# Performance work log

Hardware: AMD Instinct MI355X
Metric: run time of the kernel (lower is better)

## Reference

```python
import jax, jax.numpy as jnp
import numpy as np

K = 8      # neighbors (from __init__ default k=8)
EPS = 1e-5 # BatchNorm1d default eps


def conv1x1(x, w, b):
    # x: (B,C,N), w: (O,C), b: (O,) -> (B,O,N)
    return jnp.einsum('bcn,oc->bon', x, w) + b[None, :, None]


def batchnorm(x, g, be):
    # training-mode BatchNorm1d: stats over (B, N) per channel
    m = x.mean(axis=(0, 2), keepdims=True)
    v = x.var(axis=(0, 2), keepdims=True)
    return g[None, :, None] * (x - m) * jax.lax.rsqrt(v + EPS) + be[None, :, None]


def block(x, w, b, g, be):
    return jax.nn.relu(batchnorm(conv1x1(x, w, b), g, be))


def setup_inputs() -> dict:
    key = jax.random.key(0)
    ks = jax.random.split(key, 24)
    B, N = 16, 4096
    rn = lambda k, s, sc=0.1: jax.random.normal(k, s, jnp.float32) * sc
    ones_n = lambda k, s: jnp.ones(s, jnp.float32) + rn(k, s, 0.01)
    return {
        'points': jax.random.normal(ks[0], (B, N, 3), jnp.float32),
        'w1': rn(ks[1], (64, 3)),   'b1': rn(ks[2], (64,)),
        'g1': ones_n(ks[3], (64,)), 'be1': rn(ks[4], (64,)),
        'w3': rn(ks[5], (512, 64)), 'b3': rn(ks[6], (512,)),
        'g3': ones_n(ks[7], (512,)), 'be3': rn(ks[8], (512,)),
        'hw1': rn(ks[9], (512, 1088)), 'hb1': rn(ks[10], (512,)),
        'hg1': ones_n(ks[11], (512,)), 'hbe1': rn(ks[12], (512,)),
        'hw2': rn(ks[13], (256, 512)), 'hb2': rn(ks[14], (256,)),
        'hg2': ones_n(ks[15], (256,)), 'hbe2': rn(ks[16], (256,)),
        'hw3': rn(ks[17], (128, 256)), 'hb3': rn(ks[18], (128,)),
        'hg3': ones_n(ks[19], (128,)), 'hbe3': rn(ks[20], (128,)),
        'hw4': rn(ks[21], (6, 128)), 'hb4': rn(ks[22], (6,)),
    }


def reference(points, w1, b1, g1, be1, w3, b3, g3, be3,
              hw1, hb1, hg1, hbe1, hw2, hb2, hg2, hbe2,
              hw3, hb3, hg3, hbe3, hw4, hb4):
    B, N, _ = points.shape
    # brute-force KNN (squared L2, ascending -> top_k on -dist)
    x2 = jnp.sum(points * points, axis=-1)                     # (B,N)
    dist = x2[:, :, None] + x2[:, None, :] \
        - 2.0 * jnp.einsum('bnd,bmd->bnm', points, points)      # (B,N,N)
    idx = jax.lax.top_k(-dist, K)[1]                           # (B,N,K) int32

    p = points.transpose(0, 2, 1)                              # (B,3,N)
    l_feat = block(p, w1, b1, g1, be1)                         # (B,64,N)
    x = block(l_feat, w3, b3, g3, be3)                         # (B,512,N)
    x_t = x.transpose(0, 2, 1)                                 # (B,N,512)

    # Faithful to the original's gather bug:
    # out[b,n,k,c] = x_t[b, idx[b,n,k], k]  (independent of c since K<512)
    vals = jnp.take_along_axis(x_t[:, :, :K], idx, axis=1)     # (B,N,K)
    m = vals.max(axis=2)                                       # (B,N)
    local_features = jnp.broadcast_to(m[:, None, :], (B, 512, N))

    global_feat = jnp.broadcast_to(x.max(axis=2, keepdims=True), (B, 512, N))
    h = jnp.concatenate([local_features, l_feat, global_feat], axis=1)  # (B,1088,N)
    h = block(h, hw1, hb1, hg1, hbe1)
    h = block(h, hw2, hb2, hg2, hbe2)
    h = block(h, hw3, hb3, hg3, hbe3)
    h = conv1x1(h, hw4, hb4)                                   # (B,6,N)
    return h.transpose(0, 2, 1)                                # (B,N,6)
```

## Files before the change

### kernel.cpp

```cpp
#include <hip/hip_runtime.h>
#include <hip/hip_bf16.h>
#include <math.h>

typedef __attribute__((ext_vector_type(8))) short short8;
typedef __attribute__((ext_vector_type(16))) float f32x16;

__device__ inline f32x16 mfma32(short8 a, short8 b, f32x16 c) {
    return __builtin_amdgcn_mfma_f32_32x32x16_bf16(a, b, c, 0, 0, 0);
}

__device__ inline void bsplit(float x, ushort& h, ushort& l) {
    __hip_bfloat16 bh = __float2bfloat16(x);
    float hf = __bfloat162float(bh);
    __hip_bfloat16 bl = __float2bfloat16(x - hf);
    h = *reinterpret_cast<ushort*>(&bh);
    l = *reinterpret_cast<ushort*>(&bl);
}

__device__ inline float unmap_f(unsigned int mp) {
    unsigned int db = mp ^ (0x80000000u | (unsigned int)((int)(~mp) >> 31));
    return __uint_as_float(db);
}

__global__ void k_wsplit_all(
    const float* __restrict__ w3s, const float* __restrict__ hw1,
    const float* __restrict__ hw2, const float* __restrict__ hw3,
    const float* __restrict__ hw4,
    ushort* __restrict__ w3h, ushort* __restrict__ w3l,
    ushort* __restrict__ w1eh, ushort* __restrict__ w1el,
    ushort* __restrict__ w2h, ushort* __restrict__ w2l,
    ushort* __restrict__ wh3h, ushort* __restrict__ wh3l,
    ushort* __restrict__ w4h, ushort* __restrict__ w4l) {
    int i = blockIdx.x * 256 + threadIdx.x;
    const float* src; int rs, co, Ms, K, base; ushort *hi, *lo;
    if (i < 32768)       { src = w3s; rs = 64;   co = 0;   Ms = 512; K = 64;  hi = w3h;  lo = w3l;  base = 0; }
    else if (i < 65536)  { src = hw1; rs = 1088; co = 512; Ms = 512; K = 64;  hi = w1eh; lo = w1el; base = 32768; }
    else if (i < 196608) { src = hw2; rs = 512;  co = 0;   Ms = 256; K = 512; hi = w2h;  lo = w2l;  base = 65536; }
    else if (i < 229376) { src = hw3; rs = 256;  co = 0;   Ms = 128; K = 256; hi = wh3h; lo = wh3l; base = 196608; }
    else if (i < 233472) { src = hw4; rs = 128;  co = 0;   Ms = 6;   K = 128; hi = w4h;  lo = w4l;  base = 229376; }
    else return;
    int li = i - base;
    int o = li / K, k = li - o * K;
    float x = (o < Ms) ? src[(size_t)o * rs + co + k] : 0.f;
    ushort h, l;
    bsplit(x, h, l);
    hi[li] = h; lo[li] = l;
}

__global__ void k_stats1(const float* __restrict__ pts, const float* __restrict__ w1,
                         const float* __restrict__ b1, float* __restrict__ part1) {
    __shared__ float sw[256];
    __shared__ float wred[2][4][64];
    int t = threadIdx.x;
    if (t < 192) sw[t] = w1[t];
    if (t < 64) sw[192 + t] = b1[t];
    __syncthreads();
    int g = blockIdx.x * 256 + t;
    float p0 = pts[g*3], p1 = pts[g*3+1], p2 = pts[g*3+2];
    int lane = t & 63, wv = t >> 6;
    for (int c = 0; c < 64; c++) {
        float y = fmaf(sw[c*3+2], p2, fmaf(sw[c*3+1], p1, fmaf(sw[c*3], p0, sw[192+c])));
        float s = y, q = y * y;
        #pragma unroll
        for (int o = 32; o > 0; o >>= 1) { s += __shfl_down(s, o); q += __shfl_down(q, o); }
        if (lane == 0) { wred[0][wv][c] = s; wred[1][wv][c] = q; }
    }
    __syncthreads();
    if (t < 64) {
        float s = wred[0][0][t] + wred[0][1][t] + wred[0][2][t] + wred[0][3][t];
        float q = wred[1][0][t] + wred[1][1][t] + wred[1][2][t] + wred[1][3][t];
        part1[blockIdx.x * 128 + t] = s;
        part1[blockIdx.x * 128 + 64 + t] = q;
    }
}

__global__ void k_fin(const float* __restrict__ part, int count, int stride, int sqoff,
                      const float* __restrict__ g, const float* __restrict__ be,
                      float* __restrict__ sout, float* __restrict__ tout) {
    int c = blockIdx.x, t = threadIdx.x;
    float s = 0.f, q = 0.f;
    for (int w = t; w < count; w += 256) { s += part[(size_t)w*stride + c]; q += part[(size_t)w*stride + sqoff + c]; }
    __shared__ float rs[4], rq[4];
    int lane = t & 63, wv = t >> 6;
    #pragma unroll
    for (int o = 32; o > 0; o >>= 1) { s += __shfl_down(s, o); q += __shfl_down(q, o); }
    if (lane == 0) { rs[wv] = s; rq[wv] = q; }
    __syncthreads();
    if (t == 0) {
        s = rs[0] + rs[1] + rs[2] + rs[3];
        q = rq[0] + rq[1] + rq[2] + rq[3];
        float mean = s / 65536.f;
        float var = q / 65536.f - mean * mean;
        float sc = g[c] * rsqrtf(var + 1e-5f);
        sout[c] = sc;
        tout[c] = be[c] - mean * sc;
    }
}

__global__ void k_lfeat2(const float* __restrict__ pts, const float* __restrict__ w1,
                         const float* __restrict__ b1, const float* __restrict__ s1,
                         const float* __restrict__ t1, ushort* __restrict__ lfh,
                         ushort* __restrict__ lfl) {
    __shared__ float sw[256], ss[64], st[64];
    int t = threadIdx.x;
    if (t < 192) sw[t] = w1[t];
    if (t < 64) { sw[192+t] = b1[t]; ss[t] = s1[t]; st[t] = t1[t]; }
    __syncthreads();
    int g = blockIdx.x * 256 + t;
    float p0 = pts[g*3], p1 = pts[g*3+1], p2 = pts[g*3+2];
    for (int c0 = 0; c0 < 64; c0 += 8) {
        union { short8 v; ushort u[8]; } H, L;
        #pragma unroll
        for (int j = 0; j < 8; j++) {
            int c = c0 + j;
            float y = fmaf(sw[c*3+2], p2, fmaf(sw[c*3+1], p1, fmaf(sw[c*3], p0, sw[192+c])));
            float a = fmaxf(fmaf(ss[c], y, st[c]), 0.f);
            bsplit(a, H.u[j], L.u[j]);
        }
        *(short8*)(lfh + (size_t)g*64 + c0) = H.v;
        *(short8*)(lfl + (size_t)g*64 + c0) = L.v;
    }
}

template<int MODE>
__global__ __launch_bounds__(256, 2) void k_gemm64(
    const ushort* __restrict__ Bhi, const ushort* __restrict__ Blo,
    const ushort* __restrict__ Ahi, const ushort* __restrict__ Alo,
    const float* __restrict__ bias, const float* __restrict__ A1,
    const float* __restrict__ G1, const float* __restrict__ mb,
    float* __restrict__ part, float* __restrict__ y38) {
    __shared__ ushort sbh[128*64], sbl[128*64];
    __shared__ float sPb[512], sPa[512];
    int t = threadIdx.x, pb = blockIdx.x;
    int gn0 = pb * 128, b = pb >> 5;
    for (int i = t; i < 512; i += 256) {
        float bb = bias[i];
        if (MODE) bb += G1[(b<<9) + i];
        sPb[i] = bb;
        sPa[i] = MODE ? A1[i] : 0.f;
    }
    for (int it = 0; it < 4; it++) {
        int s = it*256 + t;
        int n = s >> 3, c16 = s & 7;
        int off = (c16*16) ^ ((n & 7) << 4);
        int sb8 = (it*256 + (t & 192)) * 8;
        __builtin_amdgcn_global_load_lds((const char*)Bhi + (size_t)(gn0+n)*128 + off, &sbh[sb8], 16, 0, 0);
        __builtin_amdgcn_global_load_lds((const char*)Blo + (size_t)(gn0+n)*128 + off, &sbl[sb8], 16, 0, 0);
    }
    __syncthreads();
    int lane = t & 63, wv = t >> 6, m = lane & 31, kg = lane >> 5;
    for (int ct = 0; ct < 4; ct++) {
        int ch0 = wv*128 + ct*32;
        short8 ah[4], al[4];
        #pragma unroll
        for (int ks = 0; ks < 4; ks++) {
            ah[ks] = *(const short8*)(Ahi + (size_t)(ch0+m)*64 + ks*16 + kg*8);
            al[ks] = *(const short8*)(Alo + (size_t)(ch0+m)*64 + ks*16 + kg*8);
        }
        float ssum[16] = {}, ssq[16] = {}, smx[16];
        #pragma unroll
        for (int r = 0; r < 16; r++) smx[r] = -__builtin_inff();
        for (int pt = 0; pt < 4; pt++) {
            int n = pt*32 + m;
            f32x16 acc = {};
            #pragma unroll
            for (int ks = 0; ks < 4; ks++) {
                int off = ((ks*16 + kg*8)*2) ^ ((n & 7) << 4);
                short8 bh = *(const short8*)((const char*)sbh + n*128 + off);
                short8 bl = *(const short8*)((const char*)sbl + n*128 + off);
                acc = mfma32(ah[ks], bh, acc);
                acc = mfma32(ah[ks], bl, acc);
                acc = mfma32(al[ks], bh, acc);
            }
            float mval = MODE ? mb[gn0 + n] : 0.f;
            #pragma unroll
            for (int r = 0; r < 16; r++) {
                int chr = ch0 + (r&3) + 8*(r>>2) + 4*kg;
                float v = acc[r] + sPb[chr] + (MODE ? sPa[chr]*mval : 0.f);
                ssum[r] += v; ssq[r] = fmaf(v, v, ssq[r]);
                if (MODE == 0) {
                    smx[r] = fmaxf(smx[r], v);
                    if (wv == 0 && ct == 0 && r < 4) {
                        int c8 = (r&3) + 4*kg;
                        y38[(size_t)c8*65536 + gn0 + n] = v;
                    }
                }
            }
        }
        #pragma unroll
        for (int r = 0; r < 16; r++) {
            float s = ssum[r], q = ssq[r], x = smx[r];
            #pragma unroll
            for (int o = 16; o > 0; o >>= 1) {
                s += __shfl_xor(s, o); q += __shfl_xor(q, o);
                if (MODE == 0) x = fmaxf(x, __shfl_xor(x, o));
            }
            if (m == 0) {
                int chr = ch0 + (r&3) + 8*(r>>2) + 4*kg;
                if (MODE == 0) {
                    part[(size_t)pb*1536 + chr] = s;
                    part[(size_t)pb*1536 + 512 + chr] = q;
                    part[(size_t)pb*1536 + 1024 + chr] = x;
                } else {
                    part[(size_t)pb*1024 + chr] = s;
                    part[(size_t)pb*1024 + 512 + chr] = q;
                }
            }
        }
    }
}

__global__ void k_fin3b(const float* __restrict__ part3, const float* __restrict__ s3,
                        const float* __restrict__ t3, float* __restrict__ gmaxb) {
    int b = blockIdx.x, c = threadIdx.x;
    float mx = -__builtin_inff();
    for (int i = 0; i < 32; i++) mx = fmaxf(mx, part3[(size_t)(b*32+i)*1536 + 1024 + c]);
    gmaxb[(b<<9)+c] = fmaxf(fmaf(s3[c], mx, t3[c]), 0.f);
}

__global__ void k_a1g1(const float* __restrict__ hw1, const float* __restrict__ gmaxb,
                       float* __restrict__ A1, float* __restrict__ G1) {
    __shared__ float sg[512];
    int blk = blockIdx.x, t = threadIdx.x;
    if (blk < 32) {
        int b = blk >> 1;
        for (int i = t; i < 512; i += 256) sg[i] = gmaxb[(b<<9)+i];
        __syncthreads();
        int o = (blk & 1)*256 + t;
        float s = 0.f;
        for (int c4 = 0; c4 < 128; c4++) {
            float4 w = *(const float4*)&hw1[(size_t)o*1088 + 576 + c4*4];
            s = fmaf(w.x, sg[c4*4],   s);
            s = fmaf(w.y, sg[c4*4+1], s);
            s = fmaf(w.z, sg[c4*4+2], s);
            s = fmaf(w.w, sg[c4*4+3], s);
        }
        G1[(b<<9)+o] = s;
    } else {
        int o = (blk - 32)*256 + t;
        float s = 0.f;
        for (int c4 = 0; c4 < 128; c4++) {
            float4 w = *(const float4*)&hw1[(size_t)o*1088 + c4*4];
            s += w.x; s += w.y; s += w.z; s += w.w;
        }
        A1[o] = s;
    }
}

__global__ __launch_bounds__(1024, 8)
void k_knn(const float* __restrict__ pts, const float* __restrict__ y38,
           const float* __restrict__ s3, const float* __restrict__ t3,
           float* __restrict__ mbuf) {
    __shared__ float4 sp[4096];
    int t = threadIdx.x, blk = blockIdx.x;
    int b = blk >> 5;
    int lane = t & 63, wv = t >> 6;
    const float* pb = pts + (size_t)b * 4096 * 3;
    for (int i = t; i < 4096; i += 1024) {
        float c0 = pb[i*3], c1 = pb[i*3+1], c2 = pb[i*3+2];
        float cw = __fadd_rn(__fadd_rn(__fmul_rn(c0,c0), __fmul_rn(c1,c1)), __fmul_rn(c2,c2));
        sp[i] = make_float4(c0, c1, c2, cw);
    }
    __syncthreads();
    const int NINF = 0xff800000;
    int qbase = (blk & 31) * 128 + wv * 8;
    for (int qi = 0; qi < 8; qi++) {
        int nq = qbase + qi;
        float4 qp = sp[nq];
        float q0 = qp.x, q1 = qp.y, q2 = qp.z, qx2 = qp.w;
        float sd; unsigned int si;
        {
            float4 cp = sp[lane];
            float dot = __fadd_rn(__fadd_rn(__fmul_rn(q0,cp.x), __fmul_rn(q1,cp.y)), __fmul_rn(q2,cp.z));
            float d = __fsub_rn(__fadd_rn(qx2, cp.w), __fmul_rn(2.f, dot));
            unsigned int db = __float_as_uint(d);
            unsigned int mp = db ^ (0x80000000u | (unsigned int)((int)db >> 31));
            unsigned long long key = ((unsigned long long)mp << 32) | (unsigned int)lane;
            #pragma unroll
            for (int k = 2; k <= 64; k <<= 1) {
                #pragma unroll
                for (int jj = k >> 1; jj >= 1; jj >>= 1) {
                    unsigned long long pk = __shfl_xor(key, jj);
                    bool up = ((lane & k) == 0);
                    bool lower = ((lane & jj) == 0);
                    bool keepmin = (lower == up);
                    unsigned long long mn = (pk < key) ? pk : key;
                    unsigned long long mx = (pk < key) ? key : pk;
                    key = keepmin ? mn : mx;
                }
            }
            sd = unmap_f((unsigned int)(key >> 32));
            si = (unsigned int)key;
        }
        float thr = __shfl(sd, 7);
        for (int j = 1; j < 64; j++) {
            float4 cp = sp[j*64 + lane];
            float dot = __fadd_rn(__fadd_rn(__fmul_rn(q0,cp.x), __fmul_rn(q1,cp.y)), __fmul_rn(q2,cp.z));
            float d = __fsub_rn(__fadd_rn(qx2, cp.w), __fmul_rn(2.f, dot));
            unsigned long long mask = __ballot(d < thr);
            if (mask != 0ull) {
                do {
                    int src = __ffsll(mask) - 1;
                    float db = __uint_as_float(__builtin_amdgcn_readlane(__float_as_uint(d), src));
                    unsigned int mb_ = (unsigned int)(j*64 + src);
                    float pd = __int_as_float(__builtin_amdgcn_update_dpp(
                        NINF, __float_as_int(sd), 0x111, 0xf, 0xf, false));
                    unsigned int pi = (unsigned int)__builtin_amdgcn_update_dpp(
                        0, (int)si, 0x111, 0xf, 0xf, false);
                    bool keep = (sd <= db);
                    bool pk = (pd <= db);
                    sd = keep ? sd : (pk ? db : pd);
                    si = keep ? si : (pk ? mb_ : pi);
                    mask &= (mask - 1ull);
                } while (mask != 0ull);
                thr = __shfl(sd, 7);
            }
        }
        if (lane < 8) {
            float y = y38[(size_t)lane*65536 + (b<<12) + (si & 4095)];
            float mv = fmaxf(fmaf(s3[lane], y, t3[lane]), 0.f);
            mv = fmaxf(mv, __shfl_xor(mv, 1));
            mv = fmaxf(mv, __shfl_xor(mv, 2));
            mv = fmaxf(mv, __shfl_xor(mv, 4));
            if (lane == 0) mbuf[(b<<12) + nq] = mv;
        }
    }
}

__global__ __launch_bounds__(256, 2) void k_a1w(
    const ushort* __restrict__ lfh, const ushort* __restrict__ lfl,
    const ushort* __restrict__ W1hi, const ushort* __restrict__ W1lo,
    const float* __restrict__ hb1, const float* __restrict__ A1g,
    const float* __restrict__ G1g, const float* __restrict__ mb,
    const float* __restrict__ sh1, const float* __restrict__ th1,
    ushort* __restrict__ a1hg, ushort* __restrict__ a1lg) {
    __shared__ ushort sbh[32*64], sbl[32*64];
    __shared__ ushort a1h[32*512], a1l[32*512];
    __shared__ float sP0[512], sP1[512], sSh[512];
    int t = threadIdx.x, pb = blockIdx.x;
    int gn0 = pb * 32, b = pb >> 7;
    for (int i = t; i < 512; i += 256) {
        float s = sh1[i];
        sP0[i] = fmaf(s, hb1[i] + G1g[(b<<9)+i], th1[i]);
        sP1[i] = s * A1g[i];
        sSh[i] = s;
    }
    {
        int s = t;
        int n = s >> 3, c16 = s & 7;
        int off = (c16*16) ^ ((n & 7) << 4);
        int sb8 = (t & 192) * 8;
        __builtin_amdgcn_global_load_lds((const char*)lfh + (size_t)(gn0+n)*128 + off, &sbh[sb8], 16, 0, 0);
        __builtin_amdgcn_global_load_lds((const char*)lfl + (size_t)(gn0+n)*128 + off, &sbl[sb8], 16, 0, 0);
    }
    __syncthreads();
    int lane = t & 63, wv = t >> 6, m = lane & 31, kg = lane >> 5;
    float mval = mb[gn0 + m];
    for (int ct = 0; ct < 4; ct++) {
        int ch0 = wv*128 + ct*32;
        f32x16 acc = {};
        #pragma unroll
        for (int ks = 0; ks < 4; ks++) {
            short8 ah = *(const short8*)(W1hi + (size_t)(ch0+m)*64 + ks*16 + kg*8);
            short8 al = *(const short8*)(W1lo + (size_t)(ch0+m)*64 + ks*16 + kg*8);
            int off = ((ks*16 + kg*8)*2) ^ ((m & 7) << 4);
            short8 bh = *(const short8*)((const char*)sbh + m*128 + off);
            short8 bl = *(const short8*)((const char*)sbl + m*128 + off);
            acc = mfma32(ah, bh, acc);
            acc = mfma32(ah, bl, acc);
            acc = mfma32(al, bh, acc);
        }
        #pragma unroll
        for (int q = 0; q < 4; q++) {
            ushort hs[4], ls[4];
            #pragma unroll
            for (int i = 0; i < 4; i++) {
                int r = q*4 + i;
                int chr = ch0 + i + 8*q + 4*kg;
                float a = fmaxf(fmaf(sSh[chr], acc[r], sP0[chr] + sP1[chr]*mval), 0.f);
                bsplit(a, hs[i], ls[i]);
            }
            int chb = ch0 + 8*q + 4*kg;
            int off = (chb*2) ^ ((m & 15) << 4);
            uint2 vh, vl;
            vh.x = (uint)hs[0] | ((uint)hs[1] << 16); vh.y = (uint)hs[2] | ((uint)hs[3] << 16);
            vl.x = (uint)ls[0] | ((uint)ls[1] << 16); vl.y = (uint)ls[2] | ((uint)ls[3] << 16);
            *(uint2*)((char*)a1h + m*1024 + off) = vh;
            *(uint2*)((char*)a1l + m*1024 + off) = vl;
        }
    }
    __syncthreads();
    for (int i = t; i < 2048; i += 256) {
        int p = i >> 6, c16 = i & 63;
        int off = (c16*16) ^ ((p & 15) << 4);
        *(uint4*)(a1hg + (size_t)(gn0+p)*512 + c16*8) = *(const uint4*)((const char*)a1h + p*1024 + off);
        *(uint4*)(a1lg + (size_t)(gn0+p)*512 + c16*8) = *(const uint4*)((const char*)a1l + p*1024 + off);
    }
}

__global__ __launch_bounds__(256, 2) void k_h2g(
    const ushort* __restrict__ a1hg, const ushort* __restrict__ a1lg,
    const ushort* __restrict__ W2hi, const ushort* __restrict__ W2lo,
    const float* __restrict__ hb2,
    float* __restrict__ pre2, float* __restrict__ parth2) {
    __shared__ ushort sbh[128*128], sbl[128*128];
    int t = threadIdx.x, pb = blockIdx.x;
    int gn0 = pb * 128;
    int lane = t & 63, wv = t >> 6, m = lane & 31, kg = lane >> 5;
    f32x16 acc0[4] = {}, acc1[4] = {};
    for (int kc = 0; kc < 4; kc++) {
        if (kc) __syncthreads();
        #pragma unroll
        for (int it = 0; it < 8; it++) {
            int s = it*256 + t;
            int n = s >> 4, c16 = s & 15;
            int off = (c16*16) ^ ((n & 15) << 4);
            int sb8 = (it*256 + (t & 192)) * 8;
            __builtin_amdgcn_global_load_lds((const char*)a1hg + (size_t)(gn0+n)*1024 + kc*256 + off, &sbh[sb8], 16, 0, 0);
            __builtin_amdgcn_global_load_lds((const char*)a1lg + (size_t)(gn0+n)*1024 + kc*256 + off, &sbl[sb8], 16, 0, 0);
        }
        __syncthreads();
        for (int ks = 0; ks < 8; ks++) {
            int ko = ks*16 + kg*8;
            int kglob = kc*128 + ko;
            short8 w0h = *(const short8*)(W2hi + (size_t)(wv*64+m)*512 + kglob);
            short8 w0l = *(const short8*)(W2lo + (size_t)(wv*64+m)*512 + kglob);
            short8 w1h = *(const short8*)(W2hi + (size_t)(wv*64+32+m)*512 + kglob);
            short8 w1l = *(const short8*)(W2lo + (size_t)(wv*64+32+m)*512 + kglob);
            #pragma unroll
            for (int pt = 0; pt < 4; pt++) {
                int n = pt*32 + m;
                int off = (ko*2) ^ ((n & 15) << 4);
                short8 bh = *(const short8*)((const char*)sbh + n*256 + off);
                short8 bl = *(const short8*)((const char*)sbl + n*256 + off);
                acc0[pt] = mfma32(w0h, bh, acc0[pt]);
                acc1[pt] = mfma32(w1h, bh, acc1[pt]);
                acc0[pt] = mfma32(w0h, bl, acc0[pt]);
                acc1[pt] = mfma32(w1h, bl, acc1[pt]);
                acc0[pt] = mfma32(w0l, bh, acc0[pt]);
                acc1[pt] = mfma32(w1l, bh, acc1[pt]);
            }
        }
    }
    #pragma unroll
    for (int ti = 0; ti < 2; ti++) {
        #pragma unroll
        for (int r = 0; r < 16; r++) {
            int chr = wv*64 + ti*32 + (r&3) + 8*(r>>2) + 4*kg;
            float hb = hb2[chr];
            float s = 0.f, q = 0.f;
            #pragma unroll
            for (int pt = 0; pt < 4; pt++) {
                float v = (ti ? acc1[pt][r] : acc0[pt][r]) + hb;
                pre2[(size_t)chr*65536 + gn0 + pt*32 + m] = v;
                s += v; q = fmaf(v, v, q);
            }
            #pragma unroll
            for (int o = 16; o > 0; o >>= 1) { s += __shfl_xor(s, o); q += __shfl_xor(q, o); }
            if (m == 0) {
                parth2[(size_t)pb*512 + chr] = s;
                parth2[(size_t)pb*512 + 256 + chr] = q;
            }
        }
    }
}

__global__ __launch_bounds__(256, 2) void k_h3s(
    const float* __restrict__ pre2, const float* __restrict__ sh2,
    const float* __restrict__ th2,
    const ushort* __restrict__ W3hi, const ushort* __restrict__ W3lo,
    const float* __restrict__ hb3, float* __restrict__ parth3) {
    __shared__ ushort sbh[32*256], sbl[32*256];
    __shared__ float ft[128*36];
    __shared__ float sS2[256], sT2[256];
    int t = threadIdx.x, pb = blockIdx.x;
    sS2[t] = sh2[t]; sT2[t] = th2[t];
    int lane = t & 63, wv = t >> 6, m = lane & 31, kg = lane >> 5;
    int ch0 = wv * 32;
    int cn = t & 31, cgq = t >> 5;
    float bhr[16];
    #pragma unroll
    for (int r = 0; r < 16; r++) bhr[r] = hb3[ch0 + (r&3) + 8*(r>>2) + 4*kg];
    float ssum[16] = {}, ssq[16] = {};
    for (int pt = 0; pt < 4; pt++) {
        int gn0 = pb*128 + pt*32;
        for (int h = 0; h < 2; h++) {
            __syncthreads();
            #pragma unroll
            for (int i = 0; i < 4; i++) {
                int idx = i*256 + t;
                int row = idx >> 3, c4 = idx & 7;
                float4 v = *(const float4*)(pre2 + (size_t)(h*128+row)*65536 + gn0 + c4*4);
                float* dst = &ft[row*36 + c4*4];
                dst[0] = v.x; dst[1] = v.y; dst[2] = v.z; dst[3] = v.w;
            }
            __syncthreads();
            #pragma unroll
            for (int i4 = 0; i4 < 4; i4++) {
                int cl0 = cgq*16 + i4*4;
                int cg0 = h*128 + cl0;
                ushort hs[4], ls[4];
                #pragma unroll
                for (int i = 0; i < 4; i++) {
                    float v = fmaxf(fmaf(sS2[cg0+i], ft[(cl0+i)*36 + cn], sT2[cg0+i]), 0.f);
                    bsplit(v, hs[i], ls[i]);
                }
                int off = cn*512 + (((cg0 >> 3)*16) ^ ((cn & 15) << 4)) + (cg0 & 7)*2;
                uint2 vh, vl;
                vh.x = (uint)hs[0] | ((uint)hs[1] << 16); vh.y = (uint)hs[2] | ((uint)hs[3] << 16);
                vl.x = (uint)ls[0] | ((uint)ls[1] << 16); vl.y = (uint)ls[2] | ((uint)ls[3] << 16);
                *(uint2*)((char*)sbh + off) = vh;
                *(uint2*)((char*)sbl + off) = vl;
            }
        }
        __syncthreads();
        f32x16 acc = {};
        for (int ks = 0; ks < 16; ks++) {
            int ko = ks*16 + kg*8;
            int off = (ko*2) ^ ((m & 15) << 4);
            short8 bh = *(const short8*)((const char*)sbh + m*512 + off);
            short8 bl = *(const short8*)((const char*)sbl + m*512 + off);
            short8 ah = *(const short8*)(W3hi + (size_t)(ch0+m)*256 + ko);
            short8 al = *(const short8*)(W3lo + (size_t)(ch0+m)*256 + ko);
            acc = mfma32(ah, bh, acc);
            acc = mfma32(ah, bl, acc);
            acc = mfma32(al, bh, acc);
        }
        #pragma unroll
        for (int r = 0; r < 16; r++) {
            float v = acc[r] + bhr[r];
            ssum[r] += v; ssq[r] = fmaf(v, v, ssq[r]);
        }
    }
    #pragma unroll
    for (int r = 0; r < 16; r++) {
        float s = ssum[r], q = ssq[r];
        #pragma unroll
        for (int o = 16; o > 0; o >>= 1) { s += __shfl_xor(s, o); q += __shfl_xor(q, o); }
        if (m == 0) {
            int chr = ch0 + (r&3) + 8*(r>>2) + 4*kg;
            parth3[(size_t)pb*256 + chr] = s;
            parth3[(size_t)pb*256 + 128 + chr] = q;
        }
    }
}

__global__ __launch_bounds__(256, 2) void k_h4m(
    const float* __restrict__ pre2, const float* __restrict__ sh2,
    const float* __restrict__ th2,
    const ushort* __restrict__ W3hi, const ushort* __restrict__ W3lo,
    const float* __restrict__ hb3, const float* __restrict__ sh3,
    const float* __restrict__ th3, const ushort* __restrict__ W4hi,
    const ushort* __restrict__ W4lo, const float* __restrict__ hb4,
    float* __restrict__ out) {
    __shared__ ushort sbh[32*256], sbl[32*256];
    __shared__ float ft[128*36];
    __shared__ float sS[128], sT[128], sB[128];
    __shared__ float sS2[256], sT2[256];
    ushort* a3h = (ushort*)ft;
    ushort* a3l = ((ushort*)ft) + 32*128;
    int t = threadIdx.x, pb = blockIdx.x;
    int gn0 = pb * 32;
    if (t < 128) { sS[t] = sh3[t]; sT[t] = th3[t]; sB[t] = hb3[t]; }
    sS2[t] = sh2[t]; sT2[t] = th2[t];
    int cn = t & 31, cgq = t >> 5;
    for (int h = 0; h < 2; h++) {
        __syncthreads();
        #pragma unroll
        for (int i = 0; i < 4; i++) {
            int idx = i*256 + t;
            int row = idx >> 3, c4 = idx & 7;
            float4 v = *(const float4*)(pre2 + (size_t)(h*128+row)*65536 + gn0 + c4*4);
            float* dst = &ft[row*36 + c4*4];
            dst[0] = v.x; dst[1] = v.y; dst[2] = v.z; dst[3] = v.w;
        }
        __syncthreads();
        #pragma unroll
        for (int i4 = 0; i4 < 4; i4++) {
            int cl0 = cgq*16 + i4*4;
            int cg0 = h*128 + cl0;
            ushort hs[4], ls[4];
            #pragma unroll
            for (int i = 0; i < 4; i++) {
                float v = fmaxf(fmaf(sS2[cg0+i], ft[(cl0+i)*36 + cn], sT2[cg0+i]), 0.f);
                bsplit(v, hs[i], ls[i]);
            }
            int off = cn*512 + (((cg0 >> 3)*16) ^ ((cn & 15) << 4)) + (cg0 & 7)*2;
            uint2 vh, vl;
            vh.x = (uint)hs[0] | ((uint)hs[1] << 16); vh.y = (uint)hs[2] | ((uint)hs[3] << 16);
            vl.x = (uint)ls[0] | ((uint)ls[1] << 16); vl.y = (uint)ls[2] | ((uint)ls[3] << 16);
            *(uint2*)((char*)sbh + off) = vh;
            *(uint2*)((char*)sbl + off) = vl;
        }
    }
    __syncthreads();
    int lane = t & 63, wv = t >> 6, m = lane & 31, kg = lane >> 5;
    int ch0 = wv * 32;
    f32x16 acc = {};
    for (int ks = 0; ks < 16; ks++) {
        int ko = ks*16 + kg*8;
        int off = (ko*2) ^ ((m & 15) << 4);
        short8 bh = *(const short8*)((const char*)sbh + m*512 + off);
        short8 bl = *(const short8*)((const char*)sbl + m*512 + off);
        short8 ah = *(const short8*)(W3hi + (size_t)(ch0+m)*256 + ko);
        short8 al = *(const short8*)(W3lo + (size_t)(ch0+m)*256 + ko);
        acc = mfma32(ah, bh, acc);
        acc = mfma32(ah, bl, acc);
        acc = mfma32(al, bh, acc);
    }
    #pragma unroll
    for (int q = 0; q < 4; q++) {
        ushort hs[4], ls[4];
        #pragma unroll
        for (int i = 0; i < 4; i++) {
            int r = q*4 + i;
            int chr = ch0 + i + 8*q + 4*kg;
            float v = fmaxf(fmaf(sS[chr], acc[r] + sB[chr], sT[chr]), 0.f);
            bsplit(v, hs[i], ls[i]);
        }
        int chb = ch0 + 8*q + 4*kg;
        int off = (chb*2) ^ ((m & 15) << 4);
        uint2 vh, vl;
        vh.x = (uint)hs[0] | ((uint)hs[1] << 16); vh.y = (uint)hs[2] | ((uint)hs[3] << 16);
        vl.x = (uint)ls[0] | ((uint)ls[1] << 16); vl.y = (uint)ls[2] | ((uint)ls[3] << 16);
        *(uint2*)((char*)a3h + m*256 + off) = vh;
        *(uint2*)((char*)a3l + m*256 + off) = vl;
    }
    __syncthreads();
    if (wv == 0) {
        f32x16 acc2 = {};
        for (int ks = 0; ks < 8; ks++) {
            int ko = ks*16 + kg*8;
            int off = (ko*2) ^ ((m & 15) << 4);
            short8 bh = *(const short8*)((const char*)a3h + m*256 + off);
            short8 bl = *(const short8*)((const char*)a3l + m*256 + off);
            short8 ah = *(const short8*)(W4hi + (size_t)m*128 + ko);
            short8 al = *(const short8*)(W4lo + (size_t)m*128 + ko);
            acc2 = mfma32(ah, bh, acc2);
            acc2 = mfma32(ah, bl, acc2);
            acc2 = mfma32(al, bh, acc2);
        }
        #pragma unroll
        for (int r = 0; r < 16; r++) {
            int mrow = (r&3) + 8*(r>>2) + 4*kg;
            if (mrow < 6) out[(size_t)(gn0+m)*6 + mrow] = acc2[r] + hb4[mrow];
        }
    }
}

extern "C" void kernel_launch(void* const* d_in, const int* in_sizes, int n_in,
                              void* d_out, int out_size, void* d_ws, size_t ws_size,
                              hipStream_t stream) {
    const float* pts  = (const float*)d_in[0];
    const float* w1   = (const float*)d_in[1];
    const float* b1   = (const float*)d_in[2];
    const float* g1   = (const float*)d_in[3];
    const float* be1  = (const float*)d_in[4];
    const float* w3   = (const float*)d_in[5];
    const float* b3   = (const float*)d_in[6];
    const float* g3   = (const float*)d_in[7];
    const float* be3  = (const float*)d_in[8];
    const float* hw1  = (const float*)d_in[9];
    const float* hb1  = (const float*)d_in[10];
    const float* hg1  = (const float*)d_in[11];
    const float* hbe1 = (const float*)d_in[12];
    const float* hw2  = (const float*)d_in[13];
    const float* hb2  = (const float*)d_in[14];
    const float* hg2  = (const float*)d_in[15];
    const float* hbe2 = (const float*)d_in[16];
    const float* hw3  = (const float*)d_in[17];
    const float* hb3  = (const float*)d_in[18];
    const float* hg3  = (const float*)d_in[19];
    const float* hbe3 = (const float*)d_in[20];
    const float* hw4  = (const float*)d_in[21];
    const float* hb4  = (const float*)d_in[22];
    (void)in_sizes; (void)n_in; (void)out_size; (void)ws_size;

    float* W = (float*)d_ws;
    size_t off = 0;
    auto alloc = [&](size_t n) { float* p = W + off; off += n; return p; };
    auto allocU = [&](size_t nshorts) { return (ushort*)alloc((nshorts + 1) / 2); };

    ushort* lfh  = allocU(65536UL*64);
    ushort* lfl  = allocU(65536UL*64);
    ushort* a1hg = allocU(65536UL*512);
    ushort* a1lg = allocU(65536UL*512);
    ushort* w3h  = allocU(512*64);  ushort* w3l  = allocU(512*64);
    ushort* w1eh = allocU(512*64);  ushort* w1el = allocU(512*64);
    ushort* w2h  = allocU(256*512); ushort* w2l  = allocU(256*512);
    ushort* wh3h = allocU(128*256); ushort* wh3l = allocU(128*256);
    ushort* w4h  = allocU(32*128);  ushort* w4l  = allocU(32*128);
    float* y38    = alloc(524288);
    float* mbuf   = alloc(65536);
    float* gmaxb  = alloc(8192);
    float* G1     = alloc(8192);
    float* A1     = alloc(512);
    float* s1 = alloc(64);  float* t1 = alloc(64);
    float* s3 = alloc(512); float* t3 = alloc(512);
    float* sh1 = alloc(512); float* th1 = alloc(512);
    float* sh2 = alloc(256); float* th2 = alloc(256);
    float* sh3 = alloc(128); float* th3 = alloc(128);
    float* part1  = alloc(32768);
    float* part3  = alloc(512*1536);
    float* parth1 = alloc(512*1024);
    float* parth2 = alloc(512*512);
    float* parth3 = alloc(512*256);
    float* pre2   = alloc(16777216);

    k_wsplit_all<<<912, 256, 0, stream>>>(w3, hw1, hw2, hw3, hw4,
                                          w3h, w3l, w1eh, w1el, w2h, w2l,
                                          wh3h, wh3l, w4h, w4l);

    k_stats1<<<256, 256, 0, stream>>>(pts, w1, b1, part1);
    k_fin<<<64, 256, 0, stream>>>(part1, 256, 128, 64, g1, be1, s1, t1);
    k_lfeat2<<<256, 256, 0, stream>>>(pts, w1, b1, s1, t1, lfh, lfl);
    k_gemm64<0><<<512, 256, 0, stream>>>(lfh, lfl, w3h, w3l, b3, nullptr, nullptr, nullptr, part3, y38);
    k_fin<<<512, 256, 0, stream>>>(part3, 512, 1536, 512, g3, be3, s3, t3);
    k_fin3b<<<16, 512, 0, stream>>>(part3, s3, t3, gmaxb);
    k_a1g1<<<34, 256, 0, stream>>>(hw1, gmaxb, A1, G1);
    k_knn<<<512, 1024, 0, stream>>>(pts, y38, s3, t3, mbuf);
    k_gemm64<1><<<512, 256, 0, stream>>>(lfh, lfl, w1eh, w1el, hb1, A1, G1, mbuf, parth1, nullptr);
    k_fin<<<512, 256, 0, stream>>>(parth1, 512, 1024, 512, hg1, hbe1, sh1, th1);
    k_a1w<<<2048, 256, 0, stream>>>(lfh, lfl, w1eh, w1el, hb1, A1, G1, mbuf, sh1, th1, a1hg, a1lg);
    k_h2g<<<512, 256, 0, stream>>>(a1hg, a1lg, w2h, w2l, hb2, pre2, parth2);
    k_fin<<<256, 256, 0, stream>>>(parth2, 512, 512, 256, hg2, hbe2, sh2, th2);
    k_h3s<<<512, 256, 0, stream>>>(pre2, sh2, th2, wh3h, wh3l, hb3, parth3);
    k_fin<<<128, 256, 0, stream>>>(parth3, 512, 256, 128, hg3, hbe3, sh3, th3);
    k_h4m<<<2048, 256, 0, stream>>>(pre2, sh2, th2, wh3h, wh3l, hb3, sh3, th3, w4h, w4l, hb4, (float*)d_out);
}
```

Before: 487.0 us.

## Fuse head layer-1 activation recompute into layer-2 GEMM, drop a1 round trip

Merges the kernel that recomputed and wrote the 512-channel layer-1 activations (as bf16 hi/lo splits) with the layer-2 GEMM. Each block now computes 64-channel chunks of the activation into shared memory and feeds them straight into the W2 MFMAs, so the 2x64MB global write and read of a1 are gone. The price is extra __syncthreads per chunk and the layer-1 MFMA work serialized within the same block, which lowers overlap and adds LDS traffic.

```diff
diff --git a/kernel.cpp b/kernel.cpp
--- a/kernel.cpp
+++ b/kernel.cpp
@@ -327,102 +327,79 @@
     }
 }
 
-__global__ __launch_bounds__(256, 2) void k_a1w(
+__global__ __launch_bounds__(256, 2) void k_h2f(
     const ushort* __restrict__ lfh, const ushort* __restrict__ lfl,
     const ushort* __restrict__ W1hi, const ushort* __restrict__ W1lo,
+    const ushort* __restrict__ W2hi, const ushort* __restrict__ W2lo,
     const float* __restrict__ hb1, const float* __restrict__ A1g,
     const float* __restrict__ G1g, const float* __restrict__ mb,
     const float* __restrict__ sh1, const float* __restrict__ th1,
-    ushort* __restrict__ a1hg, ushort* __restrict__ a1lg) {
-    __shared__ ushort sbh[32*64], sbl[32*64];
-    __shared__ ushort a1h[32*512], a1l[32*512];
+    const float* __restrict__ hb2,
+    float* __restrict__ pre2, float* __restrict__ parth2) {
+    __shared__ ushort sLh[128*64], sLl[128*64];
+    __shared__ ushort a1h[128*64], a1l[128*64];
     __shared__ float sP0[512], sP1[512], sSh[512];
     int t = threadIdx.x, pb = blockIdx.x;
-    int gn0 = pb * 32, b = pb >> 7;
+    int gn0 = pb * 128, b = pb >> 5;
     for (int i = t; i < 512; i += 256) {
         float s = sh1[i];
         sP0[i] = fmaf(s, hb1[i] + G1g[(b<<9)+i], th1[i]);
         sP1[i] = s * A1g[i];
         sSh[i] = s;
     }
-    {
-        int s = t;
+    for (int it = 0; it < 4; it++) {
+        int s = it*256 + t;
         int n = s >> 3, c16 = s & 7;
         int off = (c16*16) ^ ((n & 7) << 4);
-        int sb8 = (t & 192) * 8;
-        __builtin_amdgcn_global_load_lds((const char*)lfh + (size_t)(gn0+n)*128 + off, &sbh[sb8], 16, 0, 0);
-        __builtin_amdgcn_global_load_lds((const char*)lfl + (size_t)(gn0+n)*128 + off, &sbl[sb8], 16, 0, 0);
+        int sb8 = (it*256 + (t & 192)) * 8;
+        __builtin_amdgcn_global_load_lds((const char*)lfh + (size_t)(gn0+n)*128 + off, &sLh[sb8], 16, 0, 0);
+        __builtin_amdgcn_global_load_lds((const char*)lfl + (size_t)(gn0+n)*128 + off, &sLl[sb8], 16, 0, 0);
     }
     __syncthreads();
     int lane = t & 63, wv = t >> 6, m = lane & 31, kg = lane >> 5;
-    float mval = mb[gn0 + m];
-    for (int ct = 0; ct < 4; ct++) {
-        int ch0 = wv*128 + ct*32;
-        f32x16 acc = {};
+    int pn = wv*32 + m;
+    float mval = mb[gn0 + pn];
+    f32x16 acc0[4] = {}, acc1[4] = {};
+    for (int ch = 0; ch < 8; ch++) {
+        #pragma unroll
+        for (int cht = 0; cht < 2; cht++) {
+            int cch = ch*64 + cht*32;
+            f32x16 acc = {};
+            #pragma unroll
+            for (int ks = 0; ks < 4; ks++) {
+                short8 ah = *(const short8*)(W1hi + (size_t)(cch+m)*64 + ks*16 + kg*8);
+                short8 al = *(const short8*)(W1lo + (size_t)(cch+m)*64 + ks*16 + kg*8);
+                int off = ((ks*16 + kg*8)*2) ^ ((m & 7) << 4);
+                short8 bh = *(const short8*)((const char*)sLh + pn*128 + off);
+                short8 bl = *(const short8*)((const char*)sLl + pn*128 + off);
+                acc = mfma32(ah, bh, acc);
+                acc = mfma32(ah, bl, acc);
+                acc = mfma32(al, bh, acc);
+            }
+            #pragma unroll
+            for (int q = 0; q < 4; q++) {
+                ushort hs[4], ls[4];
+                #pragma unroll
+                for (int i = 0; i < 4; i++) {
+                    int r = q*4 + i;
+                    int chr = cch + i + 8*q + 4*kg;
+                    float a = fmaxf(fmaf(sSh[chr], acc[r], sP0[chr] + sP1[chr]*mval), 0.f);
+                    bsplit(a, hs[i], ls[i]);
+                }
+                int chb = cht*32 + 8*q + 4*kg;
+                int off = (chb*2) ^ ((m & 7) << 4);
+                uint2 vh, vl;
+                vh.x = (uint)hs[0] | ((uint)hs[1] << 16); vh.y = (uint)hs[2] | ((uint)hs[3] << 16);
+                vl.x = (uint)ls[0] | ((uint)ls[1] << 16); vl.y = (uint)ls[2] | ((uint)ls[3] << 16);
+                *(uint2*)((char*)a1h + pn*128 + off) = vh;
+                *(uint2*)((char*)a1l + pn*128 + off) = vl;
+            }
+        }
+        __syncthreads();
         #pragma unroll
         for (int ks = 0; ks < 4; ks++) {
-            short8 ah = *(const short8*)(W1hi + (size_t)(ch0+m)*64 + ks*16 + kg*8);
-            short8 al = *(const short8*)(W1lo + (size_t)(ch0+m)*64 + ks*16 + kg*8);
-            int off = ((ks*16 + kg*8)*2) ^ ((m & 7) << 4);
-            short8 bh = *(const short8*)((const char*)sbh + m*128 + off);
-            short8 bl = *(const short8*)((const char*)sbl + m*128 + off);
-            acc = mfma32(ah, bh, acc);
-            acc = mfma32(ah, bl, acc);
-            acc = mfma32(al, bh, acc);
-        }
-        #pragma unroll
-        for (int q = 0; q < 4; q++) {
-            ushort hs[4], ls[4];
-            #pragma unroll
-            for (int i = 0; i < 4; i++) {
-                int r = q*4 + i;
-                int chr = ch0 + i + 8*q + 4*kg;
-                float a = fmaxf(fmaf(sSh[chr], acc[r], sP0[chr] + sP1[chr]*mval), 0.f);
-                bsplit(a, hs[i], ls[i]);
-            }
-            int chb = ch0 + 8*q + 4*kg;
-            int off = (chb*2) ^ ((m & 15) << 4);
-            uint2 vh, vl;
-            vh.x = (uint)hs[0] | ((uint)hs[1] << 16); vh.y = (uint)hs[2] | ((uint)hs[3] << 16);
-            vl.x = (uint)ls[0] | ((uint)ls[1] << 16); vl.y = (uint)ls[2] | ((uint)ls[3] << 16);
-            *(uint2*)((char*)a1h + m*1024 + off) = vh;
-            *(uint2*)((char*)a1l + m*1024 + off) = vl;
-        }
-    }
-    __syncthreads();
-    for (int i = t; i < 2048; i += 256) {
-        int p = i >> 6, c16 = i & 63;
-        int off = (c16*16) ^ ((p & 15) << 4);
-        *(uint4*)(a1hg + (size_t)(gn0+p)*512 + c16*8) = *(const uint4*)((const char*)a1h + p*1024 + off);
-        *(uint4*)(a1lg + (size_t)(gn0+p)*512 + c16*8) = *(const uint4*)((const char*)a1l + p*1024 + off);
-    }
-}
-
-__global__ __launch_bounds__(256, 2) void k_h2g(
-    const ushort* __restrict__ a1hg, const ushort* __restrict__ a1lg,
-    const ushort* __restrict__ W2hi, const ushort* __restrict__ W2lo,
-    const float* __restrict__ hb2,
-    float* __restrict__ pre2, float* __restrict__ parth2) {
-    __shared__ ushort sbh[128*128], sbl[128*128];
-    int t = threadIdx.x, pb = blockIdx.x;
-    int gn0 = pb * 128;
-    int lane = t & 63, wv = t >> 6, m = lane & 31, kg = lane >> 5;
-    f32x16 acc0[4] = {}, acc1[4] = {};
-    for (int kc = 0; kc < 4; kc++) {
-        if (kc) __syncthreads();
-        #pragma unroll
-        for (int it = 0; it < 8; it++) {
-            int s = it*256 + t;
-            int n = s >> 4, c16 = s & 15;
-            int off = (c16*16) ^ ((n & 15) << 4);
-            int sb8 = (it*256 + (t & 192)) * 8;
-            __builtin_amdgcn_global_load_lds((const char*)a1hg + (size_t)(gn0+n)*1024 + kc*256 + off, &sbh[sb8], 16, 0, 0);
-            __builtin_amdgcn_global_load_lds((const char*)a1lg + (size_t)(gn0+n)*1024 + kc*256 + off, &sbl[sb8], 16, 0, 0);
-        }
-        __syncthreads();
-        for (int ks = 0; ks < 8; ks++) {
-            int ko = ks*16 + kg*8;
-            int kglob = kc*128 + ko;
+            int koc = ks*16 + kg*8;
+            int kglob = ch*64 + koc;
             short8 w0h = *(const short8*)(W2hi + (size_t)(wv*64+m)*512 + kglob);
             short8 w0l = *(const short8*)(W2lo + (size_t)(wv*64+m)*512 + kglob);
             short8 w1h = *(const short8*)(W2hi + (size_t)(wv*64+32+m)*512 + kglob);
@@ -430,9 +407,9 @@
             #pragma unroll
             for (int pt = 0; pt < 4; pt++) {
                 int n = pt*32 + m;
-                int off = (ko*2) ^ ((n & 15) << 4);
-                short8 bh = *(const short8*)((const char*)sbh + n*256 + off);
-                short8 bl = *(const short8*)((const char*)sbl + n*256 + off);
+                int off = (koc*2) ^ ((n & 7) << 4);
+                short8 bh = *(const short8*)((const char*)a1h + n*128 + off);
+                short8 bl = *(const short8*)((const char*)a1l + n*128 + off);
                 acc0[pt] = mfma32(w0h, bh, acc0[pt]);
                 acc1[pt] = mfma32(w1h, bh, acc1[pt]);
                 acc0[pt] = mfma32(w0h, bl, acc0[pt]);
@@ -441,6 +418,7 @@
                 acc1[pt] = mfma32(w1l, bh, acc1[pt]);
             }
         }
+        __syncthreads();
     }
     #pragma unroll
     for (int ti = 0; ti < 2; ti++) {
@@ -683,8 +661,6 @@
 
     ushort* lfh  = allocU(65536UL*64);
     ushort* lfl  = allocU(65536UL*64);
-    ushort* a1hg = allocU(65536UL*512);
-    ushort* a1lg = allocU(65536UL*512);
     ushort* w3h  = allocU(512*64);  ushort* w3l  = allocU(512*64);
     ushort* w1eh = allocU(512*64);  ushort* w1el = allocU(512*64);
     ushort* w2h  = allocU(256*512); ushort* w2l  = allocU(256*512);
@@ -721,8 +697,8 @@
     k_knn<<<512, 1024, 0, stream>>>(pts, y38, s3, t3, mbuf);
     k_gemm64<1><<<512, 256, 0, stream>>>(lfh, lfl, w1eh, w1el, hb1, A1, G1, mbuf, parth1, nullptr);
     k_fin<<<512, 256, 0, stream>>>(parth1, 512, 1024, 512, hg1, hbe1, sh1, th1);
-    k_a1w<<<2048, 256, 0, stream>>>(lfh, lfl, w1eh, w1el, hb1, A1, G1, mbuf, sh1, th1, a1hg, a1lg);
-    k_h2g<<<512, 256, 0, stream>>>(a1hg, a1lg, w2h, w2l, hb2, pre2, parth2);
+    k_h2f<<<512, 256, 0, stream>>>(lfh, lfl, w1eh, w1el, w2h, w2l, hb1, A1, G1, mbuf,
+                                   sh1, th1, hb2, pre2, parth2);
     k_fin<<<256, 256, 0, stream>>>(parth2, 512, 512, 256, hg2, hbe2, sh2, th2);
     k_h3s<<<512, 256, 0, stream>>>(pre2, sh2, th2, wh3h, wh3l, hb3, parth3);
     k_fin<<<128, 256, 0, stream>>>(parth3, 512, 256, 128, hg3, hbe3, sh3, th3);
```

Result: faster. 457.1 us (-6.1%).
